# Optimization experiments

Measured on AMD Instinct MI355X. Metric: run time of the kernel, lower is better.

Reference implementation:

```python
import jax, jax.numpy as jnp
import numpy as np

N = 100000
E = 1600000
IN_CH = 128
OUT_CH = 512
NEG_SLOPE = 0.2
EPS = 1e-16


def _glorot(key, shape):
    fan_in, fan_out = shape[0], shape[-1]
    lim = float(np.sqrt(6.0 / (fan_in + fan_out)))
    return jax.random.uniform(key, shape, jnp.float32, -lim, lim)


def setup_inputs() -> dict:
    key = jax.random.key(0)
    ks = jax.random.split(key, 20)
    inp = {
        "x": jax.random.normal(ks[0], (N, IN_CH), jnp.float32),
        "edge_index": jax.random.randint(ks[1], (2, E), 0, N, jnp.int64),
        "edge_attr": jax.random.normal(ks[2], (E, 8), jnp.float32),
        # GATConv 1: 128 -> 32, heads=1, concat=True
        "W1": _glorot(ks[3], (IN_CH, 32)),
        "as1": _glorot(ks[4], (1, 32)),
        "ad1": _glorot(ks[5], (1, 32)),
        "b1": jnp.zeros((32,), jnp.float32),
        # GATConv 2: 32 -> 64, heads=1, concat=True
        "W2": _glorot(ks[6], (32, 64)),
        "as2": _glorot(ks[7], (1, 64)),
        "ad2": _glorot(ks[8], (1, 64)),
        "b2": jnp.zeros((64,), jnp.float32),
        # GATConv 3: 64 -> 64, heads=1, concat=False
        "W3": _glorot(ks[9], (64, 64)),
        "as3": _glorot(ks[10], (1, 64)),
        "ad3": _glorot(ks[11], (1, 64)),
        "b3": jnp.zeros((64,), jnp.float32),
        # Final Linear: 64 -> 512
        "Wl": _glorot(ks[12], (64, OUT_CH)),
        "bl": jnp.zeros((OUT_CH,), jnp.float32),
    }
    return inp


def _gat_layer(x, src, dst, W, a_src, a_dst, bias, heads, out_dim, concat):
    # Linear transform per head: [N, H, O]
    h = (x @ W).reshape(-1, heads, out_dim)
    # Per-node attention terms: [N, H]
    alpha_s = jnp.sum(h * a_src[None], axis=-1)
    alpha_d = jnp.sum(h * a_dst[None], axis=-1)
    # Edge logits with LeakyReLU: [E+N, H]
    e = jax.nn.leaky_relu(alpha_s[src] + alpha_d[dst], NEG_SLOPE)
    # Segment softmax over edges grouped by destination node
    m = jax.ops.segment_max(e, dst, num_segments=N)
    e = jnp.exp(e - m[dst])
    denom = jax.ops.segment_sum(e, dst, num_segments=N)
    alpha = e / (denom[dst] + EPS)  # [E+N, H]
    # Weighted message scatter-aggregate: [N, H, O]
    msg = h[src] * alpha[:, :, None]
    out = jax.ops.segment_sum(msg, dst, num_segments=N)
    if concat:
        out = out.reshape(-1, heads * out_dim)
    else:
        out = out.mean(axis=1)
    return out + bias


def reference(x, edge_index, edge_attr, W1, as1, ad1, b1, W2, as2, ad2, b2,
              W3, as3, ad3, b3, Wl, bl):
    # edge_dim=None -> edge_attr ignored by GATConv (lin_edge is None).
    # GATConv default add_self_loops=True: append (i, i) for every node.
    loops = jnp.arange(N, dtype=edge_index.dtype)
    src = jnp.concatenate([edge_index[0], loops])
    dst = jnp.concatenate([edge_index[1], loops])

    h = _gat_layer(x, src, dst, W1, as1, ad1, b1, heads=1, out_dim=32, concat=True)
    h = jax.nn.relu(h)
    h = _gat_layer(h, src, dst, W2, as2, ad2, b2, heads=1, out_dim=64, concat=True)
    h = jax.nn.relu(h)
    h = _gat_layer(h, src, dst, W3, as3, ad3, b3, heads=1, out_dim=64, concat=False)
    h = jax.nn.relu(h)
    return h @ Wl + bl
```

## Files before the change

kernel.cpp:

```cpp
#include <hip/hip_runtime.h>
#include <math.h>

namespace {

constexpr int NN = 100000;
constexpr int EE = 1600000;
constexpr float SLOPE = 0.2f;
constexpr float EPS_F = 1e-16f;
constexpr int NB = (NN + 255) / 256;

constexpr int NBKT = 8;
constexpr int BKT_NODES = (NN + NBKT - 1) / NBKT;
constexpr int BKT_CAP = 220000;

__device__ __forceinline__ float lrelu(float v) {
    return (v >= 0.f) ? v : SLOPE * v;
}

__device__ __forceinline__ float readlane_f(float v, int l) {
    return __uint_as_float(__builtin_amdgcn_readlane(__float_as_uint(v), l));
}

template <int IN, int OUT>
__global__ __launch_bounds__(256) void gemm_alpha(
    const float* __restrict__ x, const float* __restrict__ W,
    const float* __restrict__ avs, const float* __restrict__ avd,
    float* __restrict__ h, float* __restrict__ alps, float* __restrict__ alpd) {
    constexpr int TCg = OUT / 4;
    constexpr int TNg = 256 / TCg;
    constexpr int NODES = TNg * 4;
    constexpr int KC = 32;
    constexpr int KCP = KC + 4;
    __shared__ __align__(16) float xl[NODES * KCP];
    const int tid = threadIdx.x;
    const int tc = tid % TCg;
    const int tn = tid / TCg;
    const int n0 = blockIdx.x * NODES;
    float acc[4][4] = {};

    for (int kc = 0; kc < IN; kc += KC) {
        __syncthreads();
        for (int i = tid * 4; i < NODES * KC; i += 1024) {
            int nl = i / KC, k = i % KC;
            int gn = n0 + nl;
            float4 v = make_float4(0.f, 0.f, 0.f, 0.f);
            if (gn < NN) v = *(const float4*)&x[(size_t)gn * IN + kc + k];
            *(float4*)&xl[nl * KCP + k] = v;
        }
        __syncthreads();
        for (int k = 0; k < KC; k += 4) {
            float4 hv[4];
#pragma unroll
            for (int j = 0; j < 4; ++j)
                hv[j] = *(const float4*)&xl[(j * TNg + tn) * KCP + k];
#pragma unroll
            for (int kk = 0; kk < 4; ++kk) {
                float4 wv = *(const float4*)&W[(size_t)(kc + k + kk) * OUT + tc * 4];
#pragma unroll
                for (int j = 0; j < 4; ++j) {
                    float hk = reinterpret_cast<const float*>(&hv[j])[kk];
                    acc[j][0] += hk * wv.x;
                    acc[j][1] += hk * wv.y;
                    acc[j][2] += hk * wv.z;
                    acc[j][3] += hk * wv.w;
                }
            }
        }
    }

    const float4 avsv = *(const float4*)&avs[tc * 4];
    const float4 avdv = *(const float4*)&avd[tc * 4];
#pragma unroll
    for (int j = 0; j < 4; ++j) {
        const int gn = n0 + j * TNg + tn;
        float4 o = make_float4(acc[j][0], acc[j][1], acc[j][2], acc[j][3]);
        if (gn < NN) *(float4*)&h[(size_t)gn * OUT + tc * 4] = o;
        float vs = o.x * avsv.x + o.y * avsv.y + o.z * avsv.z + o.w * avsv.w;
        float vd = o.x * avdv.x + o.y * avdv.y + o.z * avdv.z + o.w * avdv.w;
#pragma unroll
        for (int off = TCg / 2; off > 0; off >>= 1) {
            vs += __shfl_xor(vs, off, TCg);
            vd += __shfl_xor(vd, off, TCg);
        }
        if (tc == 0 && gn < NN) {
            alps[gn] = vs;
            alpd[gn] = vd;
        }
    }
}


__global__ __launch_bounds__(256) void bin_edges(
    const int* __restrict__ ei, int* __restrict__ deg,
    int* __restrict__ cur8, unsigned int* __restrict__ pairbuf) {
    __shared__ int cnt[NBKT];
    __shared__ int base[NBKT];
    const int tid = threadIdx.x;
    for (int it = blockIdx.x; (size_t)it * 1024 < EE; it += gridDim.x) {
        const int e0 = it * 1024;
        if (tid < NBKT) cnt[tid] = 0;
        __syncthreads();
        int bk[4], lr[4];
        unsigned int pk[4];
#pragma unroll
        for (int k = 0; k < 4; ++k) {
            int e = e0 + k * 256 + tid;
            bk[k] = -1;
            if (e < EE) {
                int s = ei[e], d = ei[EE + e];
                atomicAdd(&deg[d], 1);
                int b = d / BKT_NODES;
                bk[k] = b;
                pk[k] = (unsigned)s | ((unsigned)(d - b * BKT_NODES) << 17);
                lr[k] = atomicAdd(&cnt[b], 1);
            }
        }
        __syncthreads();
        if (tid < NBKT) base[tid] = (cnt[tid] > 0) ? atomicAdd(&cur8[tid], cnt[tid]) : 0;
        __syncthreads();
#pragma unroll
        for (int k = 0; k < 4; ++k) {
            if (bk[k] >= 0) {
                int pos = base[bk[k]] + lr[k];
                if (pos < BKT_CAP)
                    pairbuf[(size_t)bk[k] * BKT_CAP + pos] = pk[k];
            }
        }
        __syncthreads();
    }
}

__global__ __launch_bounds__(256) void scan_block(int* __restrict__ offs,
                                                  int* __restrict__ bsum) {
    __shared__ int tmp[256];
    const int t = threadIdx.x;
    const int i = blockIdx.x * 256 + t;
    int v = (i < NN) ? offs[i] : 0;
    tmp[t] = v;
    __syncthreads();
    int sum = v;
    for (int off = 1; off < 256; off <<= 1) {
        int add = (t >= off) ? tmp[t - off] : 0;
        __syncthreads();
        sum += add;
        tmp[t] = sum;
        __syncthreads();
    }
    if (i < NN) offs[i] = sum - v;
    if (t == 255) bsum[blockIdx.x] = sum;
}

__global__ __launch_bounds__(512) void scan_tops(int* __restrict__ bsum) {
    __shared__ int tmp[512];
    const int t = threadIdx.x;
    int v = (t < NB) ? bsum[t] : 0;
    tmp[t] = v;
    __syncthreads();
    int sum = v;
    for (int off = 1; off < 512; off <<= 1) {
        int add = (t >= off) ? tmp[t - off] : 0;
        __syncthreads();
        sum += add;
        tmp[t] = sum;
        __syncthreads();
    }
    if (t < NB) bsum[t] = sum - v;
}

__global__ __launch_bounds__(256) void scan_add(int* __restrict__ offs,
                                                const int* __restrict__ bsum,
                                                int* __restrict__ cursor) {
    const int i = blockIdx.x * 256 + threadIdx.x;
    if (i < NN) {
        int o = offs[i] + bsum[blockIdx.x];
        offs[i] = o;
        cursor[i] = o;
    }
}

__global__ __launch_bounds__(256) void csr_scatter_bucket(
    const unsigned int* __restrict__ pairbuf, const int* __restrict__ cur8,
    int* __restrict__ cursor, int* __restrict__ csr_src) {
    const int b = blockIdx.x & 7;
    const int chunk = blockIdx.x >> 3;
    const int cnt = cur8[b];
    const unsigned int* pb = &pairbuf[(size_t)b * BKT_CAP];
    const int nbase = b * BKT_NODES;
    for (int i = chunk * 256 + threadIdx.x; i < cnt; i += 32 * 256) {
        unsigned int w = pb[i];
        int s = (int)(w & 0x1FFFFu);
        int d = nbase + (int)(w >> 17);
        int pos = atomicAdd(&cursor[d], 1);
        csr_src[pos] = s;
    }
}

template <int OUT>
__global__ __launch_bounds__(256, 8) void gat_node_agg(
    const int* __restrict__ csr_src, const int* __restrict__ offs,
    const float* __restrict__ alps, const float* __restrict__ alpd,
    const float* __restrict__ h, const float* __restrict__ bias,
    float* __restrict__ out) {
    const int lane = threadIdx.x & 63;
    const int n = blockIdx.x * 4 + (threadIdx.x >> 6);
    if (n >= NN) return;
    const int c = lane & (OUT - 1);
    const int base = offs[n];
    const int end = (n + 1 < NN) ? offs[n + 1] : EE;
    const int dg = end - base;
    const float ad = alpd[n];

    const float p_self = __expf(fminf(lrelu(alps[n] + ad), 80.f));
    float denom = p_self;
    float acc = p_self * h[(size_t)n * OUT + c];

    for (int j0 = 0; j0 < dg; j0 += 64) {
        const int myj = j0 + lane;
        int s_v = 0;
        float p_v = 0.f;
        if (myj < dg) {
            s_v = csr_src[base + myj];
            p_v = __expf(fminf(lrelu(alps[s_v] + ad), 80.f));
        }
        float ps = p_v;
#pragma unroll
        for (int off = 32; off > 0; off >>= 1) ps += __shfl_xor(ps, off, 64);
        denom += ps;
        const int lim = min(64, dg - j0);
        int j = 0;
        for (; j + 3 < lim; j += 4) {
            int s0 = __builtin_amdgcn_readlane(s_v, j);
            int s1 = __builtin_amdgcn_readlane(s_v, j + 1);
            int s2 = __builtin_amdgcn_readlane(s_v, j + 2);
            int s3 = __builtin_amdgcn_readlane(s_v, j + 3);
            float p0 = readlane_f(p_v, j);
            float p1 = readlane_f(p_v, j + 1);
            float p2 = readlane_f(p_v, j + 2);
            float p3 = readlane_f(p_v, j + 3);
            float h0 = h[(size_t)s0 * OUT + c];
            float h1 = h[(size_t)s1 * OUT + c];
            float h2 = h[(size_t)s2 * OUT + c];
            float h3 = h[(size_t)s3 * OUT + c];
            acc += p0 * h0;
            acc += p1 * h1;
            acc += p2 * h2;
            acc += p3 * h3;
        }
        for (; j < lim; ++j) {
            int s = __builtin_amdgcn_readlane(s_v, j);
            float p = readlane_f(p_v, j);
            acc += p * h[(size_t)s * OUT + c];
        }
    }
    float v = acc / (denom + EPS_F) + bias[c];
    if (lane < OUT) out[(size_t)n * OUT + c] = fmaxf(v, 0.f);
}

__global__ __launch_bounds__(256, 2) void final_linear(
    const float* __restrict__ h, const float* __restrict__ W,
    const float* __restrict__ b, float* __restrict__ out) {
    __shared__ __align__(16) float hl[128 * 68];
    __shared__ __align__(16) float wl[64 * 128];
    const int tid = threadIdx.x;
    const int tn = tid & 15;
    const int tc = tid >> 4;
    const int n0 = blockIdx.x * 128;
    const int c0 = blockIdx.y * 128;

    for (int i = tid * 4; i < 128 * 64; i += 1024) {
        int nl = i >> 6, k = i & 63;
        int gn = n0 + nl;
        float4 v = make_float4(0.f, 0.f, 0.f, 0.f);
        if (gn < NN) v = *(const float4*)&h[(size_t)gn * 64 + k];
        *(float4*)&hl[nl * 68 + k] = v;
    }
    for (int i = tid * 4; i < 64 * 128; i += 1024) {
        int k = i >> 7, cc = i & 127;
        *(float4*)&wl[i] = *(const float4*)&W[(size_t)k * 512 + c0 + cc];
    }
    __syncthreads();

    float acc[8][8] = {};
#pragma unroll 2
    for (int kq = 0; kq < 64; kq += 4) {
        float4 hv[8];
#pragma unroll
        for (int j = 0; j < 8; ++j)
            hv[j] = *(const float4*)&hl[(j * 16 + tn) * 68 + kq];
#pragma unroll
        for (int kk = 0; kk < 4; ++kk) {
            const float* wr = &wl[(kq + kk) * 128 + tc * 8];
            float4 w0 = *(const float4*)wr;
            float4 w1 = *(const float4*)(wr + 4);
#pragma unroll
            for (int j = 0; j < 8; ++j) {
                float hk = reinterpret_cast<const float*>(&hv[j])[kk];
                acc[j][0] += hk * w0.x;
                acc[j][1] += hk * w0.y;
                acc[j][2] += hk * w0.z;
                acc[j][3] += hk * w0.w;
                acc[j][4] += hk * w1.x;
                acc[j][5] += hk * w1.y;
                acc[j][6] += hk * w1.z;
                acc[j][7] += hk * w1.w;
            }
        }
    }

    const float* bp = &b[c0 + tc * 8];
    const float4 b0 = *(const float4*)bp;
    const float4 b1 = *(const float4*)(bp + 4);
#pragma unroll
    for (int j = 0; j < 8; ++j) {
        int gn = n0 + j * 16 + tn;
        if (gn < NN) {
            float* op = &out[(size_t)gn * 512 + c0 + tc * 8];
            *(float4*)op = make_float4(acc[j][0] + b0.x, acc[j][1] + b0.y,
                                       acc[j][2] + b0.z, acc[j][3] + b0.w);
            *(float4*)(op + 4) = make_float4(acc[j][4] + b1.x, acc[j][5] + b1.y,
                                             acc[j][6] + b1.z, acc[j][7] + b1.w);
        }
    }
}

}

extern "C" void kernel_launch(void* const* d_in, const int* in_sizes, int n_in,
                              void* d_out, int out_size, void* d_ws, size_t ws_size,
                              hipStream_t stream) {
    const float* x = (const float*)d_in[0];
    const int* ei = (const int*)d_in[1];
    const float* W1 = (const float*)d_in[3];
    const float* as1 = (const float*)d_in[4];
    const float* ad1 = (const float*)d_in[5];
    const float* b1 = (const float*)d_in[6];
    const float* W2 = (const float*)d_in[7];
    const float* as2 = (const float*)d_in[8];
    const float* ad2 = (const float*)d_in[9];
    const float* b2 = (const float*)d_in[10];
    const float* W3 = (const float*)d_in[11];
    const float* as3 = (const float*)d_in[12];
    const float* ad3 = (const float*)d_in[13];
    const float* b3 = (const float*)d_in[14];
    const float* Wl = (const float*)d_in[15];
    const float* bl = (const float*)d_in[16];
    float* out = (float*)d_out;

    float* ws = (float*)d_ws;
    float* hbuf = ws;
    float* xbuf = hbuf + (size_t)NN * 64;
    float* asb = xbuf + (size_t)NN * 64;
    float* adb = asb + NN;
    int* offs = (int*)(adb + NN);
    int* cursor = offs + NN;
    int* bsum = cursor + NN;
    int* csr = bsum + 512;
    int* cur8 = bsum + 504;
    unsigned int* pairbuf = (unsigned int*)hbuf;

    hipMemsetAsync(offs, 0, NN * sizeof(int), stream);
    hipMemsetAsync(cur8, 0, NBKT * sizeof(int), stream);
    bin_edges<<<256, 256, 0, stream>>>(ei, offs, cur8, pairbuf);
    scan_block<<<NB, 256, 0, stream>>>(offs, bsum);
    scan_tops<<<1, 512, 0, stream>>>(bsum);
    scan_add<<<NB, 256, 0, stream>>>(offs, bsum, cursor);
    csr_scatter_bucket<<<256, 256, 0, stream>>>(pairbuf, cur8, cursor, csr);

    gemm_alpha<128, 32><<<(NN + 127) / 128, 256, 0, stream>>>(x, W1, as1, ad1, hbuf, asb, adb);
    gat_node_agg<32><<<(NN + 3) / 4, 256, 0, stream>>>(csr, offs, asb, adb, hbuf, b1, xbuf);

    gemm_alpha<32, 64><<<(NN + 63) / 64, 256, 0, stream>>>(xbuf, W2, as2, ad2, hbuf, asb, adb);
    gat_node_agg<64><<<(NN + 3) / 4, 256, 0, stream>>>(csr, offs, asb, adb, hbuf, b2, xbuf);

    gemm_alpha<64, 64><<<(NN + 63) / 64, 256, 0, stream>>>(xbuf, W3, as3, ad3, hbuf, asb, adb);
    gat_node_agg<64><<<(NN + 3) / 4, 256, 0, stream>>>(csr, offs, asb, adb, hbuf, b3, xbuf);

    dim3 fgrid((NN + 127) / 128, 4);
    final_linear<<<fgrid, 256, 0, stream>>>(xbuf, Wl, bl, out);
}
```

Measured before the change: 793.5 us.

## Split 32-wide aggregation across half-waves, unroll 64-wide gather, stage W in LDS

The 32-channel aggregation kernel now uses both half-waves, each handling alternate neighbors, and combines them with one xor shuffle. Previously the upper 32 lanes duplicated the lower half's work. The 64-channel version unrolls its neighbor gather by 8 so more loads are in flight. gemm_alpha copies the whole weight matrix into LDS once per block, so the inner loop reads W from LDS instead of global memory. This adds up to 32KB of LDS per block, which may lower occupancy.

```diff
diff --git a/kernel.cpp b/kernel.cpp
--- a/kernel.cpp
+++ b/kernel.cpp
@@ -32,14 +32,18 @@
     constexpr int KC = 32;
     constexpr int KCP = KC + 4;
     __shared__ __align__(16) float xl[NODES * KCP];
+    __shared__ __align__(16) float wlds[IN * OUT];
     const int tid = threadIdx.x;
     const int tc = tid % TCg;
     const int tn = tid / TCg;
     const int n0 = blockIdx.x * NODES;
     float acc[4][4] = {};
 
+    for (int i = tid * 4; i < IN * OUT; i += 1024)
+        *(float4*)&wlds[i] = *(const float4*)&W[i];
+
     for (int kc = 0; kc < IN; kc += KC) {
-        __syncthreads();
+        if (kc) __syncthreads();
         for (int i = tid * 4; i < NODES * KC; i += 1024) {
             int nl = i / KC, k = i % KC;
             int gn = n0 + nl;
@@ -55,7 +59,7 @@
                 hv[j] = *(const float4*)&xl[(j * TNg + tn) * KCP + k];
 #pragma unroll
             for (int kk = 0; kk < 4; ++kk) {
-                float4 wv = *(const float4*)&W[(size_t)(kc + k + kk) * OUT + tc * 4];
+                float4 wv = *(const float4*)&wlds[(kc + k + kk) * OUT + tc * 4];
 #pragma unroll
                 for (int j = 0; j < 4; ++j) {
                     float hk = reinterpret_cast<const float*>(&hv[j])[kk];
@@ -195,8 +199,7 @@
     }
 }
 
-template <int OUT>
-__global__ __launch_bounds__(256, 8) void gat_node_agg(
+__global__ __launch_bounds__(256, 8) void gat_node_agg64(
     const int* __restrict__ csr_src, const int* __restrict__ offs,
     const float* __restrict__ alps, const float* __restrict__ alpd,
     const float* __restrict__ h, const float* __restrict__ bias,
@@ -204,7 +207,7 @@
     const int lane = threadIdx.x & 63;
     const int n = blockIdx.x * 4 + (threadIdx.x >> 6);
     if (n >= NN) return;
-    const int c = lane & (OUT - 1);
+    const int c = lane;
     const int base = offs[n];
     const int end = (n + 1 < NN) ? offs[n + 1] : EE;
     const int dg = end - base;
@@ -212,7 +215,7 @@
 
     const float p_self = __expf(fminf(lrelu(alps[n] + ad), 80.f));
     float denom = p_self;
-    float acc = p_self * h[(size_t)n * OUT + c];
+    float acc = p_self * h[(size_t)n * 64 + c];
 
     for (int j0 = 0; j0 < dg; j0 += 64) {
         const int myj = j0 + lane;
@@ -228,32 +231,97 @@
         denom += ps;
         const int lim = min(64, dg - j0);
         int j = 0;
-        for (; j + 3 < lim; j += 4) {
-            int s0 = __builtin_amdgcn_readlane(s_v, j);
-            int s1 = __builtin_amdgcn_readlane(s_v, j + 1);
-            int s2 = __builtin_amdgcn_readlane(s_v, j + 2);
-            int s3 = __builtin_amdgcn_readlane(s_v, j + 3);
-            float p0 = readlane_f(p_v, j);
-            float p1 = readlane_f(p_v, j + 1);
-            float p2 = readlane_f(p_v, j + 2);
-            float p3 = readlane_f(p_v, j + 3);
-            float h0 = h[(size_t)s0 * OUT + c];
-            float h1 = h[(size_t)s1 * OUT + c];
-            float h2 = h[(size_t)s2 * OUT + c];
-            float h3 = h[(size_t)s3 * OUT + c];
-            acc += p0 * h0;
-            acc += p1 * h1;
-            acc += p2 * h2;
-            acc += p3 * h3;
+        for (; j + 7 < lim; j += 8) {
+            int s[8];
+            float p[8], hv[8];
+#pragma unroll
+            for (int u = 0; u < 8; ++u) {
+                s[u] = __builtin_amdgcn_readlane(s_v, j + u);
+                p[u] = readlane_f(p_v, j + u);
+            }
+#pragma unroll
+            for (int u = 0; u < 8; ++u) hv[u] = h[(size_t)s[u] * 64 + c];
+#pragma unroll
+            for (int u = 0; u < 8; ++u) acc += p[u] * hv[u];
         }
         for (; j < lim; ++j) {
             int s = __builtin_amdgcn_readlane(s_v, j);
             float p = readlane_f(p_v, j);
-            acc += p * h[(size_t)s * OUT + c];
+            acc += p * h[(size_t)s * 64 + c];
         }
     }
     float v = acc / (denom + EPS_F) + bias[c];
-    if (lane < OUT) out[(size_t)n * OUT + c] = fmaxf(v, 0.f);
+    out[(size_t)n * 64 + c] = fmaxf(v, 0.f);
+}
+
+__global__ __launch_bounds__(256, 8) void gat_node_agg32(
+    const int* __restrict__ csr_src, const int* __restrict__ offs,
+    const float* __restrict__ alps, const float* __restrict__ alpd,
+    const float* __restrict__ h, const float* __restrict__ bias,
+    float* __restrict__ out) {
+    const int lane = threadIdx.x & 63;
+    const int n = blockIdx.x * 4 + (threadIdx.x >> 6);
+    if (n >= NN) return;
+    const int cl = lane & 31;
+    const int hi = lane >> 5;
+    const int base = offs[n];
+    const int end = (n + 1 < NN) ? offs[n + 1] : EE;
+    const int dg = end - base;
+    const float ad = alpd[n];
+
+    const float p_self = __expf(fminf(lrelu(alps[n] + ad), 80.f));
+    float denom = p_self;
+    float acc = hi ? 0.f : p_self * h[(size_t)n * 32 + cl];
+
+    for (int j0 = 0; j0 < dg; j0 += 64) {
+        const int myj = j0 + lane;
+        int s_v = 0;
+        float p_v = 0.f;
+        if (myj < dg) {
+            s_v = csr_src[base + myj];
+            p_v = __expf(fminf(lrelu(alps[s_v] + ad), 80.f));
+        }
+        float ps = p_v;
+#pragma unroll
+        for (int off = 32; off > 0; off >>= 1) ps += __shfl_xor(ps, off, 64);
+        denom += ps;
+        const int lim = min(64, dg - j0);
+        int j = 0;
+        for (; j + 3 < lim; j += 4) {
+            int sa0 = __builtin_amdgcn_readlane(s_v, j);
+            int sa1 = __builtin_amdgcn_readlane(s_v, j + 1);
+            int sb0 = __builtin_amdgcn_readlane(s_v, j + 2);
+            int sb1 = __builtin_amdgcn_readlane(s_v, j + 3);
+            float pa0 = readlane_f(p_v, j);
+            float pa1 = readlane_f(p_v, j + 1);
+            float pb0 = readlane_f(p_v, j + 2);
+            float pb1 = readlane_f(p_v, j + 3);
+            int sA = hi ? sa1 : sa0;
+            int sB = hi ? sb1 : sb0;
+            float pA = hi ? pa1 : pa0;
+            float pB = hi ? pb1 : pb0;
+            float hA = h[(size_t)sA * 32 + cl];
+            float hB = h[(size_t)sB * 32 + cl];
+            acc += pA * hA;
+            acc += pB * hB;
+        }
+        for (; j < lim; j += 2) {
+            int s0 = __builtin_amdgcn_readlane(s_v, j);
+            float p0 = readlane_f(p_v, j);
+            int s1 = s0;
+            float p1 = 0.f;
+            if (j + 1 < lim) {
+                s1 = __builtin_amdgcn_readlane(s_v, j + 1);
+                p1 = readlane_f(p_v, j + 1);
+            }
+            int s = hi ? s1 : s0;
+            float p = hi ? p1 : p0;
+            acc += p * h[(size_t)s * 32 + cl];
+        }
+    }
+    acc += __shfl_xor(acc, 32, 64);
+    float v = acc / (denom + EPS_F) + bias[cl];
+    if (lane < 32) out[(size_t)n * 32 + cl] = fmaxf(v, 0.f);
 }
 
 __global__ __launch_bounds__(256, 2) void final_linear(
@@ -367,13 +435,13 @@
     csr_scatter_bucket<<<256, 256, 0, stream>>>(pairbuf, cur8, cursor, csr);
 
     gemm_alpha<128, 32><<<(NN + 127) / 128, 256, 0, stream>>>(x, W1, as1, ad1, hbuf, asb, adb);
-    gat_node_agg<32><<<(NN + 3) / 4, 256, 0, stream>>>(csr, offs, asb, adb, hbuf, b1, xbuf);
+    gat_node_agg32<<<(NN + 3) / 4, 256, 0, stream>>>(csr, offs, asb, adb, hbuf, b1, xbuf);
 
     gemm_alpha<32, 64><<<(NN + 63) / 64, 256, 0, stream>>>(xbuf, W2, as2, ad2, hbuf, asb, adb);
-    gat_node_agg<64><<<(NN + 3) / 4, 256, 0, stream>>>(csr, offs, asb, adb, hbuf, b2, xbuf);
+    gat_node_agg64<<<(NN + 3) / 4, 256, 0, stream>>>(csr, offs, asb, adb, hbuf, b2, xbuf);
 
     gemm_alpha<64, 64><<<(NN + 63) / 64, 256, 0, stream>>>(xbuf, W3, as3, ad3, hbuf, asb, adb);
-    gat_node_agg<64><<<(NN + 3) / 4, 256, 0, stream>>>(csr, offs, asb, adb, hbuf, b3, xbuf);
+    gat_node_agg64<<<(NN + 3) / 4, 256, 0, stream>>>(csr, offs, asb, adb, hbuf, b3, xbuf);
 
     dim3 fgrid((NN + 127) / 128, 4);
     final_linear<<<fgrid, 256, 0, stream>>>(xbuf, Wl, bl, out);
```

After: 794.6 us. No clear change (+0.1%).
